# Performance work log

Measured on AMD Instinct MI355X. Metric: run time of the kernel, lower is better.

The kernel has to match this reference:

```python
import jax, jax.numpy as jnp
import numpy as np

BN_EPS = 1e-5
NORM_EPS = 1e-12  # F.normalize default eps


def _l2norm(v, axis):
    n = jnp.sqrt(jnp.sum(v * v, axis=axis, keepdims=True))
    return v / jnp.maximum(n, NORM_EPS)


def setup_inputs() -> dict:
    key = jax.random.key(0)
    ks = jax.random.split(key, 8)
    b, n_f, c, h, w = 2, 5, 256, 64, 64
    ck, cv = c // 8, c // 2
    x = jax.random.normal(ks[0], (b, n_f, c, h, w), dtype=jnp.float32)
    prev_mask = jax.random.uniform(ks[1], (b, n_f - 1, 1, h, w), dtype=jnp.float32)
    def xavier(k, shape):
        fan_out, fan_in = shape
        a = np.sqrt(6.0 / (fan_in + fan_out))
        return jax.random.uniform(k, shape, jnp.float32, -a, a)
    return {
        "x": x,
        "prev_mask": prev_mask,
        "qk_w": xavier(ks[2], (ck, c)),
        "qv_w": xavier(ks[3], (cv, c)),
        "mk_w": xavier(ks[4], (ck, c)),
        "mv_w": xavier(ks[5], (cv, c)),
        "sm_w": xavier(ks[6], (c, c)),
        "bn_scale": jnp.ones((c,), jnp.float32),
        "bn_bias": jnp.zeros((c,), jnp.float32),
        "bn_mean": jnp.zeros((c,), jnp.float32),
        "bn_var": jnp.ones((c,), jnp.float32),
    }


def reference(x, prev_mask, qk_w, qv_w, mk_w, mv_w, sm_w, bn_scale, bn_bias, bn_mean, bn_var):
    b, n_f, c, h, w = x.shape
    ck, cv = qk_w.shape[0], qv_w.shape[0]
    hw = h * w
    m = n_f - 1

    xq = x[:, -1]   # [b,c,h,w] query frame
    xm = x[:, :-1]  # [b,m,c,h,w] memory frames

    # 1x1 convs == channel matmuls
    query_k = jnp.einsum('bchw,oc->bohw', xq, qk_w)   # [b,ck,h,w]
    query_v = jnp.einsum('bchw,oc->bohw', xq, qv_w)   # [b,cv,h,w]
    mem_k = jnp.einsum('bmchw,oc->bmohw', xm, mk_w)   # [b,m,ck,h,w]
    mem_v = jnp.einsum('bmchw,oc->bmohw', xm, mv_w)   # [b,m,cv,h,w]

    qk = _l2norm(query_k.reshape(b, ck, hw), axis=1)          # [b,ck,hw]
    mk = _l2norm(mem_k.reshape(b, m * hw, ck)                 # note: [b,m,ck,hw]->[b,m,hw,ck] flatten
                 if False else
                 _reorder_mem_k(mem_k, b, m, ck, hw), axis=2)  # [b,m*hw,ck]

    # cosine-similarity attention over all memory pixels
    attn = jnp.einsum('bcq,bkc->bqk', qk, mk)                 # [b,hw,m*hw]
    attn = jax.nn.softmax(attn, axis=2)

    mv = mem_v.reshape(b, m, cv, hw).transpose(0, 1, 3, 2).reshape(b, m * hw, cv)
    agg = jnp.einsum('bqk,bkc->bqc', attn, mv)                # [b,hw,cv]
    agg = agg.transpose(0, 2, 1).reshape(b, cv, h, w)

    y = jnp.concatenate([query_v, agg], axis=1)               # [b,c,h,w]
    y = jnp.einsum('bchw,oc->bohw', y, sm_w)
    inv = bn_scale / jnp.sqrt(bn_var + BN_EPS)
    y = (y - bn_mean[None, :, None, None]) * inv[None, :, None, None] + bn_bias[None, :, None, None]
    y = jax.nn.relu(y)

    return jnp.concatenate([xm, y[:, None]], axis=1)          # [b,n_f,c,h,w]


def _reorder_mem_k(mem_k, b, m, ck, hw):
    # [b,m,ck,h,w] -> [b,m,ck,hw] -> [b,m,hw,ck] -> [b,m*hw,ck]
    return mem_k.reshape(b, m, ck, hw).transpose(0, 1, 3, 2).reshape(b, m * hw, ck)
```

## Files before the change

### kernel.cpp

```cpp
#include <hip/hip_runtime.h>

typedef unsigned short u16;
typedef unsigned int u32;
typedef __attribute__((ext_vector_type(8))) short short8v;
typedef __attribute__((ext_vector_type(4))) float f32x4;
typedef __attribute__((ext_vector_type(16))) float f32x16;
typedef __attribute__((ext_vector_type(2))) int i32x2;

#define B 2
#define NF 5
#define C 256
#define HW 4096
#define CV 128
#define NK 16384
#define NQ 4096

__device__ __forceinline__ u16 f2bf(float f) {
    u32 u = __float_as_uint(f);
    u32 r = (u + 0x7FFFu + ((u >> 16) & 1u)) >> 16;
    return (u16)r;
}

__device__ __forceinline__ u32 cvtpk(float lo, float hi) {
    u32 r;
    asm("v_cvt_pk_bf16_f32 %0, %1, %2" : "=v"(r) : "v"(lo), "v"(hi));
    return r;
}

__device__ __forceinline__ float exp2_raw(float x) {
    float r;
    asm("v_exp_f32 %0, %1" : "=v"(r) : "v"(x));
    return r;
}

__device__ __forceinline__ i32x2 plswap(u32 vdst, u32 src0) {
    return __builtin_amdgcn_permlane32_swap((int)vdst, (int)src0, false, false);
}

__global__ __launch_bounds__(256) void prep_k(
    const float* __restrict__ qk_w, const float* __restrict__ qv_w,
    const float* __restrict__ mk_w, const float* __restrict__ mv_w,
    const float* __restrict__ sm_w,
    const float* __restrict__ bns, const float* __restrict__ bnb,
    const float* __restrict__ bnm, const float* __restrict__ bnv,
    u16* __restrict__ wsf, float* __restrict__ bias2, u16* __restrict__ wb) {
    int bx = blockIdx.x, t = threadIdx.x;
    if (bx < 256) {
        int idx = bx * 256 + t;
        int o = idx >> 8;
        float inv = bns[o] / sqrtf(bnv[o] + 1e-5f);
        wsf[idx] = f2bf(sm_w[idx] * inv);
    } else if (bx < 576) {
        int j = (bx - 256) * 256 + t;
        int v = j / 40960, rr = j % 40960;
        int row = rr >> 8, c = rr & 255;
        float s;
        if (v == 0) s = (row < 32) ? mk_w[row * 256 + c] : mv_w[(row - 32) * 256 + c];
        else        s = (row < 32) ? qk_w[row * 256 + c] : qv_w[(row - 32) * 256 + c];
        wb[j] = f2bf(s);
    } else {
        int o = t;
        float inv = bns[o] / sqrtf(bnv[o] + 1e-5f);
        bias2[o] = bnb[o] - bnm[o] * inv;
    }
}

__global__ __launch_bounds__(256) void proj_mfma(
    const float* __restrict__ x, const u16* __restrict__ wb,
    u16* __restrict__ qkn, u16* __restrict__ mkn,
    u16* __restrict__ mvt, u16* __restrict__ U, float* __restrict__ out) {
    int bx = blockIdx.x;
    int bi = bx / 320;
    int rem = bx % 320;
    int f = rem >> 6, pt = rem & 63;
    int t = threadIdx.x, w = t >> 6, lane = t & 63;
    int l15 = lane & 15, cg = lane >> 4;
    int p = pt * 64 + w * 16 + l15;
    const float* xp = x + (((size_t)bi * NF + f) * C) * HW + p;
    const u16* wrow = wb + (size_t)((f == 4) ? 160 : 0) * 256;
    float* op = out + (((size_t)bi * NF + f) * C) * HW + p;

    f32x4 acc[10];
#pragma unroll
    for (int m = 0; m < 10; m++) acc[m] = (f32x4){0.f, 0.f, 0.f, 0.f};

    for (int k = 0; k < 8; k++) {
        float xv[8];
#pragma unroll
        for (int j = 0; j < 8; j++) xv[j] = xp[(size_t)(k * 32 + cg * 8 + j) * HW];
        if (f < 4) {
#pragma unroll
            for (int j = 0; j < 8; j++) op[(size_t)(k * 32 + cg * 8 + j) * HW] = xv[j];
        }
        short8v bfrag;
#pragma unroll
        for (int j = 0; j < 8; j++) bfrag[j] = (short)f2bf(xv[j]);
#pragma unroll
        for (int m = 0; m < 10; m++) {
            short8v afrag = *(const short8v*)(wrow + (size_t)(m * 16 + l15) * 256 + k * 32 + cg * 8);
            acc[m] = __builtin_amdgcn_mfma_f32_16x16x32_bf16(afrag, bfrag, acc[m], 0, 0, 0);
        }
    }

    float ssq = 0.f;
#pragma unroll
    for (int m = 0; m < 2; m++)
#pragma unroll
        for (int r = 0; r < 4; r++) ssq += acc[m][r] * acc[m][r];
    ssq += __shfl_xor(ssq, 16, 64);
    ssq += __shfl_xor(ssq, 32, 64);
    float rn = 1.0f / fmaxf(sqrtf(ssq), 1e-12f);

    if (f == 4) {
        float rq = rn * 1.44269504f;
        u16* kd = qkn + ((size_t)bi * NQ + p) * 32;
#pragma unroll
        for (int m = 0; m < 2; m++)
#pragma unroll
            for (int r = 0; r < 4; r++) kd[m * 16 + cg * 4 + r] = f2bf(acc[m][r] * rq);
        u16* ud = U + ((size_t)bi * HW + p) * 256;
#pragma unroll
        for (int m = 2; m < 10; m++) {
            int vo = m * 16 - 32 + cg * 4;
            union { u16 h[4]; uint2 v; } pk;
#pragma unroll
            for (int r = 0; r < 4; r++) pk.h[r] = f2bf(acc[m][r]);
            *(uint2*)(ud + vo) = pk.v;
        }
    } else {
        u16* kd = mkn + ((size_t)bi * NK + f * HW + p) * 32;
#pragma unroll
        for (int m = 0; m < 2; m++)
#pragma unroll
            for (int r = 0; r < 4; r++) kd[m * 16 + cg * 4 + r] = f2bf(acc[m][r] * rn);
#pragma unroll
        for (int m = 2; m < 10; m++)
#pragma unroll
            for (int r = 0; r < 4; r++) {
                int vo = m * 16 - 32 + cg * 4 + r;
                mvt[((size_t)bi * CV + vo) * NK + f * HW + p] = f2bf(acc[m][r]);
            }
    }
}

__global__ __launch_bounds__(256, 2) void attn_k(
    const u16* __restrict__ qkn, const u16* __restrict__ mkn,
    const u16* __restrict__ mvt, u16* __restrict__ opart,
    float* __restrict__ lpart, int kc) {
    __shared__ alignas(16) u16 kl[2][64 * 40];
    __shared__ alignas(16) u16 vl[2][128 * 72];

    int bx = blockIdx.x;
    int bi = bx / (32 * kc);
    int rem = bx % (32 * kc);
    int qt = rem / kc, kci = rem % kc;
    int chunk = NK / kc, iters = chunk / 64;
    int tid = threadIdx.x, w = tid >> 6, lane = tid & 63;
    int l31 = lane & 31, hi = lane >> 5;

    int qrow = qt * 128 + w * 32 + l31;
    const u16* qp = qkn + ((size_t)bi * NQ + qrow) * 32;
    short8v qf0 = *(const short8v*)(qp + hi * 8);
    short8v qf1 = *(const short8v*)(qp + 16 + hi * 8);

    f32x16 O[4];
#pragma unroll
    for (int n = 0; n < 4; n++)
#pragma unroll
        for (int i = 0; i < 16; i++) O[n][i] = 0.f;
    float ls[4] = {0.f, 0.f, 0.f, 0.f};

    const u16* mknb = mkn + (size_t)bi * NK * 32;
    const u16* mvtb = mvt + (size_t)bi * CV * NK;
    int krow = tid >> 2, kcol = tid & 3;
    int klsoff = krow * 40 + kcol * 8;
    int vrow[4], vcol[4], vlsoff[4];
#pragma unroll
    for (int r = 0; r < 4; r++) {
        int cidx = tid + 256 * r;
        vrow[r] = cidx >> 3; vcol[r] = cidx & 7;
        vlsoff[r] = vrow[r] * 72 + vcol[r] * 8;
    }

    const u16* kptr = mknb + (size_t)(kci * chunk + krow) * 32 + kcol * 8;
    const u16* vptr[4];
#pragma unroll
    for (int r = 0; r < 4; r++)
        vptr[r] = mvtb + (size_t)vrow[r] * NK + kci * chunk + vcol[r] * 8;

    short8v kreg = *(const short8v*)kptr;
    short8v vreg[4];
#pragma unroll
    for (int r = 0; r < 4; r++) vreg[r] = *(const short8v*)vptr[r];

    int c = 0;
    for (int it = 0; it < iters; ++it) {
        *(short8v*)(&kl[c][0] + klsoff) = kreg;
#pragma unroll
        for (int r = 0; r < 4; r++) *(short8v*)(&vl[c][0] + vlsoff[r]) = vreg[r];
        if (it + 1 < iters) {
            kptr += 64 * 32;
            kreg = *(const short8v*)kptr;
#pragma unroll
            for (int r = 0; r < 4; r++) {
                vptr[r] += 64;
                vreg[r] = *(const short8v*)vptr[r];
            }
        }
        __syncthreads();
        const u16* klr = &kl[c][0];
        const u16* vlr = &vl[c][0];
#pragma unroll
        for (int t = 0; t < 2; t++) {
            int ar = t * 32 + l31;
            const u16* kb = klr + ar * 40;
            short8v ka0 = *(const short8v*)(kb + hi * 8);
            short8v ka1 = *(const short8v*)(kb + (2 + hi) * 8);
            f32x16 st;
#pragma unroll
            for (int i = 0; i < 16; i++) st[i] = 0.f;
            __builtin_amdgcn_s_setprio(1);
            st = __builtin_amdgcn_mfma_f32_32x32x16_bf16(ka0, qf0, st, 0, 0, 0);
            st = __builtin_amdgcn_mfma_f32_32x32x16_bf16(ka1, qf1, st, 0, 0, 0);
            __builtin_amdgcn_s_setprio(0);
            float p[16];
#pragma unroll
            for (int i = 0; i < 16; i++) p[i] = exp2_raw(st[i]);
#pragma unroll
            for (int g = 0; g < 4; g++)
                ls[g] += ((p[4 * g] + p[4 * g + 1]) + (p[4 * g + 2] + p[4 * g + 3]));
            u32 c0[4], c1[4];
#pragma unroll
            for (int g = 0; g < 4; g++) {
                c0[g] = cvtpk(p[4 * g], p[4 * g + 1]);
                c1[g] = cvtpk(p[4 * g + 2], p[4 * g + 3]);
            }
#pragma unroll
            for (int half = 0; half < 2; half++) {
                i32x2 s0 = plswap(c0[2 * half + 1], c0[2 * half]);
                i32x2 s1 = plswap(c1[2 * half + 1], c1[2 * half]);
                union { u32 wd[4]; short8v v; } bu;
                bu.wd[0] = (u32)s0[1];
                bu.wd[1] = (u32)s1[1];
                bu.wd[2] = (u32)s0[0];
                bu.wd[3] = (u32)s1[0];
                int kk = 2 * t + half;
                __builtin_amdgcn_s_setprio(1);
#pragma unroll
                for (int n = 0; n < 4; n++) {
                    int vr = n * 32 + l31;
                    short8v va = *(const short8v*)(vlr + vr * 72 + (kk * 2 + hi) * 8);
                    O[n] = __builtin_amdgcn_mfma_f32_32x32x16_bf16(va, bu.v, O[n], 0, 0, 0);
                }
                __builtin_amdgcn_s_setprio(0);
            }
        }
        c ^= 1;
    }

    float lsum = (ls[0] + ls[1]) + (ls[2] + ls[3]);
    lsum += __shfl_xor(lsum, 32, 64);
    uint2* op2 = (uint2*)opart;
    size_t pbase4 = (size_t)(bi * kc + kci) * 32;
#pragma unroll
    for (int n = 0; n < 4; n++)
#pragma unroll
        for (int g = 0; g < 4; g++) {
            uint2 val;
            val.x = cvtpk(O[n][4 * g + 0], O[n][4 * g + 1]);
            val.y = cvtpk(O[n][4 * g + 2], O[n][4 * g + 3]);
            int v4 = n * 8 + 2 * g + hi;
            op2[(pbase4 + v4) * NQ + qrow] = val;
        }
    if (hi == 0) lpart[(size_t)(bi * kc + kci) * NQ + qrow] = lsum;
}

__global__ __launch_bounds__(256) void combine_k(
    const u16* __restrict__ opart, const float* __restrict__ lpart,
    u16* __restrict__ U, int kc) {
    int bx = blockIdx.x;
    int bi = bx >> 7;
    int qb = ((bx >> 1) & 63) << 6;
    int vh = bx & 1;
    int t = threadIdx.x;
    int q = qb + (t & 63);
    int v40 = vh * 16 + (t >> 6) * 4;
    const uint2* op2 = (const uint2*)opart;
    float acc[16];
#pragma unroll
    for (int i = 0; i < 16; i++) acc[i] = 0.f;
    float lsum = 0.f;
    for (int k = 0; k < kc; k++) {
        size_t base4 = (size_t)(bi * kc + k) * 32 + v40;
#pragma unroll
        for (int j = 0; j < 4; j++) {
            uint2 d = op2[(base4 + j) * NQ + q];
            acc[4 * j + 0] += __uint_as_float(d.x << 16);
            acc[4 * j + 1] += __uint_as_float(d.x & 0xFFFF0000u);
            acc[4 * j + 2] += __uint_as_float(d.y << 16);
            acc[4 * j + 3] += __uint_as_float(d.y & 0xFFFF0000u);
        }
        lsum += lpart[(size_t)(bi * kc + k) * NQ + q];
    }
    float r = 1.0f / lsum;
    u16* ud = U + ((size_t)bi * HW + q) * 256 + 128 + v40 * 4;
    union { u16 h[8]; short8v v; } a, b;
#pragma unroll
    for (int e = 0; e < 8; e++) a.h[e] = f2bf(acc[e] * r);
#pragma unroll
    for (int e = 0; e < 8; e++) b.h[e] = f2bf(acc[8 + e] * r);
    *(short8v*)ud = a.v;
    *(short8v*)(ud + 8) = b.v;
}

__global__ __launch_bounds__(256) void final_mfma(
    const u16* __restrict__ U, const u16* __restrict__ wsf,
    const float* __restrict__ bias2, float* __restrict__ out) {
    int bx = blockIdx.x;
    int bi = bx >> 7;
    int mh = (bx >> 6) & 1;
    int pt = bx & 63;
    int t = threadIdx.x, w = t >> 6, lane = t & 63;
    int l15 = lane & 15, cg = lane >> 4;
    int p = pt * 64 + w * 16 + l15;
    const u16* urow = U + ((size_t)bi * HW + p) * 256;
    const u16* wbase = wsf + (size_t)mh * 128 * 256;
    f32x4 acc[8];
#pragma unroll
    for (int m = 0; m < 8; m++) acc[m] = (f32x4){0.f, 0.f, 0.f, 0.f};
    for (int k = 0; k < 8; k++) {
        short8v bfrag = *(const short8v*)(urow + k * 32 + cg * 8);
#pragma unroll
        for (int m = 0; m < 8; m++) {
            short8v afrag = *(const short8v*)(wbase + (size_t)(m * 16 + l15) * 256 + k * 32 + cg * 8);
            acc[m] = __builtin_amdgcn_mfma_f32_16x16x32_bf16(afrag, bfrag, acc[m], 0, 0, 0);
        }
    }
    float* obase = out + (((size_t)bi * NF + 4) * C) * HW;
#pragma unroll
    for (int m = 0; m < 8; m++) {
#pragma unroll
        for (int r = 0; r < 4; r++) {
            int o = mh * 128 + m * 16 + cg * 4 + r;
            obase[(size_t)o * HW + p] = fmaxf(acc[m][r] + bias2[o], 0.f);
        }
    }
}

extern "C" void kernel_launch(void* const* d_in, const int* in_sizes, int n_in,
                              void* d_out, int out_size, void* d_ws, size_t ws_size,
                              hipStream_t stream) {
    const float* x    = (const float*)d_in[0];
    const float* qk_w = (const float*)d_in[2];
    const float* qv_w = (const float*)d_in[3];
    const float* mk_w = (const float*)d_in[4];
    const float* mv_w = (const float*)d_in[5];
    const float* sm_w = (const float*)d_in[6];
    const float* bns  = (const float*)d_in[7];
    const float* bnb  = (const float*)d_in[8];
    const float* bnm  = (const float*)d_in[9];
    const float* bnv  = (const float*)d_in[10];
    float* out = (float*)d_out;
    char* ws = (char*)d_ws;

    size_t off = 0;
    auto alloc = [&](size_t bytes) { size_t o = off; off += (bytes + 255) & ~(size_t)255; return o; };
    size_t WSF = alloc(256 * 256 * 2);
    size_t BIA = alloc(256 * 4);
    size_t WB  = alloc(2 * 160 * 256 * 2);
    size_t QKN = alloc((size_t)B * NQ * 32 * 2);
    size_t MKN = alloc((size_t)B * NK * 32 * 2);
    size_t MVT = alloc((size_t)B * CV * NK * 2);
    size_t UBU = alloc((size_t)B * HW * 256 * 2);
    size_t fixed = off;
    int kc = 16;
    {
        auto need = [&](int k) {
            return fixed + (size_t)B * k * NQ * 4 + (size_t)B * k * (size_t)CV * NQ * 2 + 1024;
        };
        if (ws_size < need(16)) kc = 8;
    }
    size_t LP = alloc((size_t)B * kc * NQ * 4);
    size_t OP = alloc((size_t)B * kc * (size_t)CV * NQ * 2);

    prep_k<<<577, 256, 0, stream>>>(qk_w, qv_w, mk_w, mv_w, sm_w, bns, bnb, bnm, bnv,
        (u16*)(ws + WSF), (float*)(ws + BIA), (u16*)(ws + WB));
    proj_mfma<<<640, 256, 0, stream>>>(x, (u16*)(ws + WB),
        (u16*)(ws + QKN), (u16*)(ws + MKN), (u16*)(ws + MVT), (u16*)(ws + UBU), out);
    attn_k<<<B * 32 * kc, 256, 0, stream>>>((u16*)(ws + QKN), (u16*)(ws + MKN),
        (u16*)(ws + MVT), (u16*)(ws + OP), (float*)(ws + LP), kc);
    combine_k<<<256, 256, 0, stream>>>((u16*)(ws + OP), (float*)(ws + LP),
        (u16*)(ws + UBU), kc);
    final_mfma<<<256, 256, 0, stream>>>((u16*)(ws + UBU), (u16*)(ws + WSF),
        (float*)(ws + BIA), out);
}
```

Before: 110.1 us.

## Fuse split-K combine into final projection kernel via shared-memory aggregate tile

Merges the split-K partial combine and the final 1x1 conv + BN + ReLU into one kernel. Each block reduces the bf16 partial outputs and softmax denominators for 32 query pixels, normalizes them, and stages the aggregated values in LDS. It then runs the MFMA projection, reading the query_v half from global memory and the aggregate half from LDS. This drops one launch and the global write/read round-trip of the aggregate, at the cost of a smaller per-block pixel tile and 256 blocks covering all 256 output channels each.

```diff
diff --git a/kernel.cpp b/kernel.cpp
--- a/kernel.cpp
+++ b/kernel.cpp
@@ -275,76 +275,87 @@
     if (hi == 0) lpart[(size_t)(bi * kc + kci) * NQ + qrow] = lsum;
 }
 
-__global__ __launch_bounds__(256) void combine_k(
+__global__ __launch_bounds__(256) void final_fused(
     const u16* __restrict__ opart, const float* __restrict__ lpart,
-    u16* __restrict__ U, int kc) {
+    const u16* __restrict__ U, const u16* __restrict__ wsf,
+    const float* __restrict__ bias2, float* __restrict__ out, int kc) {
+    __shared__ alignas(16) u16 aggL[32][136];
+    __shared__ float lsumL[32];
+
     int bx = blockIdx.x;
     int bi = bx >> 7;
-    int qb = ((bx >> 1) & 63) << 6;
-    int vh = bx & 1;
+    int q0 = (bx & 127) * 32;
     int t = threadIdx.x;
-    int q = qb + (t & 63);
-    int v40 = vh * 16 + (t >> 6) * 4;
+    int px = t & 31, qs = t >> 5;
+
+    if (qs == 0) {
+        float s = 0.f;
+        for (int k = 0; k < kc; k++) s += lpart[(size_t)(bi * kc + k) * NQ + q0 + px];
+        lsumL[px] = 1.0f / s;
+    }
     const uint2* op2 = (const uint2*)opart;
-    float acc[16];
-#pragma unroll
-    for (int i = 0; i < 16; i++) acc[i] = 0.f;
-    float lsum = 0.f;
+    float s[4][4];
+#pragma unroll
+    for (int j = 0; j < 4; j++)
+#pragma unroll
+        for (int e = 0; e < 4; e++) s[j][e] = 0.f;
     for (int k = 0; k < kc; k++) {
-        size_t base4 = (size_t)(bi * kc + k) * 32 + v40;
+        size_t kb = (size_t)(bi * kc + k) * 32;
 #pragma unroll
         for (int j = 0; j < 4; j++) {
-            uint2 d = op2[(base4 + j) * NQ + q];
-            acc[4 * j + 0] += __uint_as_float(d.x << 16);
-            acc[4 * j + 1] += __uint_as_float(d.x & 0xFFFF0000u);
-            acc[4 * j + 2] += __uint_as_float(d.y << 16);
-            acc[4 * j + 3] += __uint_as_float(d.y & 0xFFFF0000u);
-        }
-        lsum += lpart[(size_t)(bi * kc + k) * NQ + q];
-    }
-    float r = 1.0f / lsum;
-    u16* ud = U + ((size_t)bi * HW + q) * 256 + 128 + v40 * 4;
-    union { u16 h[8]; short8v v; } a, b;
-#pragma unroll
-    for (int e = 0; e < 8; e++) a.h[e] = f2bf(acc[e] * r);
-#pragma unroll
-    for (int e = 0; e < 8; e++) b.h[e] = f2bf(acc[8 + e] * r);
-    *(short8v*)ud = a.v;
-    *(short8v*)(ud + 8) = b.v;
-}
-
-__global__ __launch_bounds__(256) void final_mfma(
-    const u16* __restrict__ U, const u16* __restrict__ wsf,
-    const float* __restrict__ bias2, float* __restrict__ out) {
-    int bx = blockIdx.x;
-    int bi = bx >> 7;
-    int mh = (bx >> 6) & 1;
-    int pt = bx & 63;
-    int t = threadIdx.x, w = t >> 6, lane = t & 63;
+            uint2 d = op2[(kb + qs * 4 + j) * NQ + q0 + px];
+            s[j][0] += __uint_as_float(d.x << 16);
+            s[j][1] += __uint_as_float(d.x & 0xFFFF0000u);
+            s[j][2] += __uint_as_float(d.y << 16);
+            s[j][3] += __uint_as_float(d.y & 0xFFFF0000u);
+        }
+    }
+    __syncthreads();
+    float r = lsumL[px];
+#pragma unroll
+    for (int j = 0; j < 4; j++) {
+        uint2 v;
+        v.x = cvtpk(s[j][0] * r, s[j][1] * r);
+        v.y = cvtpk(s[j][2] * r, s[j][3] * r);
+        *(uint2*)(&aggL[px][(qs * 4 + j) * 4]) = v;
+    }
+    __syncthreads();
+
+    int w = t >> 6, lane = t & 63;
     int l15 = lane & 15, cg = lane >> 4;
-    int p = pt * 64 + w * 16 + l15;
-    const u16* urow = U + ((size_t)bi * HW + p) * 256;
-    const u16* wbase = wsf + (size_t)mh * 128 * 256;
-    f32x4 acc[8];
-#pragma unroll
-    for (int m = 0; m < 8; m++) acc[m] = (f32x4){0.f, 0.f, 0.f, 0.f};
-    for (int k = 0; k < 8; k++) {
-        short8v bfrag = *(const short8v*)(urow + k * 32 + cg * 8);
-#pragma unroll
-        for (int m = 0; m < 8; m++) {
-            short8v afrag = *(const short8v*)(wbase + (size_t)(m * 16 + l15) * 256 + k * 32 + cg * 8);
-            acc[m] = __builtin_amdgcn_mfma_f32_16x16x32_bf16(afrag, bfrag, acc[m], 0, 0, 0);
+    f32x4 acc[4][2];
+#pragma unroll
+    for (int m = 0; m < 4; m++)
+#pragma unroll
+        for (int n = 0; n < 2; n++) acc[m][n] = (f32x4){0.f, 0.f, 0.f, 0.f};
+    const u16* ub = U + ((size_t)bi * HW + q0) * 256;
+    for (int k8 = 0; k8 < 8; k8++) {
+        short8v bfrag[2];
+#pragma unroll
+        for (int n = 0; n < 2; n++) {
+            int pxr = n * 16 + l15;
+            if (k8 < 4) bfrag[n] = *(const short8v*)(ub + (size_t)pxr * 256 + k8 * 32 + cg * 8);
+            else        bfrag[n] = *(const short8v*)(&aggL[pxr][(k8 - 4) * 32 + cg * 8]);
+        }
+#pragma unroll
+        for (int m = 0; m < 4; m++) {
+            short8v afrag = *(const short8v*)(wsf + (size_t)(w * 64 + m * 16 + l15) * 256 + k8 * 32 + cg * 8);
+#pragma unroll
+            for (int n = 0; n < 2; n++)
+                acc[m][n] = __builtin_amdgcn_mfma_f32_16x16x32_bf16(afrag, bfrag[n], acc[m][n], 0, 0, 0);
         }
     }
     float* obase = out + (((size_t)bi * NF + 4) * C) * HW;
 #pragma unroll
-    for (int m = 0; m < 8; m++) {
-#pragma unroll
-        for (int r = 0; r < 4; r++) {
-            int o = mh * 128 + m * 16 + cg * 4 + r;
-            obase[(size_t)o * HW + p] = fmaxf(acc[m][r] + bias2[o], 0.f);
-        }
-    }
+    for (int m = 0; m < 4; m++)
+#pragma unroll
+        for (int n = 0; n < 2; n++)
+#pragma unroll
+            for (int rr = 0; rr < 4; rr++) {
+                int o = w * 64 + m * 16 + cg * 4 + rr;
+                int px2 = n * 16 + l15;
+                obase[(size_t)o * HW + q0 + px2] = fmaxf(acc[m][n][rr] + bias2[o], 0.f);
+            }
 }
 
 extern "C" void kernel_launch(void* const* d_in, const int* in_sizes, int n_in,
@@ -389,8 +400,6 @@
         (u16*)(ws + QKN), (u16*)(ws + MKN), (u16*)(ws + MVT), (u16*)(ws + UBU), out);
     attn_k<<<B * 32 * kc, 256, 0, stream>>>((u16*)(ws + QKN), (u16*)(ws + MKN),
         (u16*)(ws + MVT), (u16*)(ws + OP), (float*)(ws + LP), kc);
-    combine_k<<<256, 256, 0, stream>>>((u16*)(ws + OP), (float*)(ws + LP),
-        (u16*)(ws + UBU), kc);
-    final_mfma<<<256, 256, 0, stream>>>((u16*)(ws + UBU), (u16*)(ws + WSF),
-        (float*)(ws + BIA), out);
-}
+    final_fused<<<256, 256, 0, stream>>>((u16*)(ws + OP), (float*)(ws + LP),
+        (u16*)(ws + UBU), (u16*)(ws + WSF), (float*)(ws + BIA), out, kc);
+}
```

Result: faster. 107.7 us (median of 2 runs) (-2.2%).
